# Kernel optimization log

Hardware: AMD Instinct MI355X
Metric: run time of the kernel (lower is better)

The kernel has to match this reference:

```python
import jax, jax.numpy as jnp
import numpy as np

# Module config (from init_kwargs)
RES = 64          # resolution
C = 8             # in_channels
NB = 64           # n_basis
CORE = 32         # core_size (edge of core cube on every axis)
POS = (RES - CORE) // 2  # periphery_size = 16; placement offset on each axis
DIM = CORE * CORE * CORE * C  # 262144
BATCH = 32


def setup_inputs() -> dict:
    key = jax.random.key(0)
    k_z, k_u = jax.random.split(key, 2)
    z = jax.random.normal(k_z, (BATCH, NB), dtype=jnp.float32)
    # SubspaceLayer params: U (n_basis, dim) orthogonal-init surrogate (random normal,
    # scaled like an orthonormal row basis), L = [3*n_basis, ..., 3] descending, mu zeros.
    U = jax.random.normal(k_u, (NB, DIM), dtype=jnp.float32) / np.sqrt(DIM)
    L = jnp.asarray([3.0 * i for i in range(NB, 0, -1)], dtype=jnp.float32)
    mu = jnp.zeros((DIM,), dtype=jnp.float32)
    return {"z": z, "U": U, "L": L, "mu": mu}


def reference(z, U, L, mu):
    # SubspaceLayer: (L * z) @ U + mu  -> (B, DIM)
    proj = (L * z) @ U + mu
    block = proj.reshape(-1, C, CORE, CORE, CORE)  # (B, C, 32, 32, 32)
    # einsum 'bcijk,id,jh,kw->bcdhw' with one-hot position matrices ==
    # place block into zero (B, C, RES, RES, RES) grid at offset POS per axis.
    b = block.shape[0]
    out = jnp.zeros((b, C, RES, RES, RES), dtype=block.dtype)
    out = out.at[:, :, POS:POS + CORE, POS:POS + CORE, POS:POS + CORE].set(block)
    return out
```

## Files before the change

### kernel.cpp

```cpp
#include <hip/hip_runtime.h>

#define BATCH 32
#define NB    64
#define CH    8
#define CORE  32
#define RES   64
#define POS   16
#define DIM   (CORE*CORE*CORE*CH)
#define OUT_PER_B (CH*RES*RES*RES)

#define CORE_BLOCKS (DIM/256)
#define ZERO_BLOCKS ((BATCH*OUT_PER_B/4)/256)

__global__ void prep_s_kernel(const float* __restrict__ z,
                              const float* __restrict__ L,
                              float* __restrict__ st) {
    int t = threadIdx.x;
#pragma unroll
    for (int r = 0; r < 8; ++r) {
        int idx = r * 256 + t;
        int k = idx >> 5;
        int b = idx & 31;
        st[idx] = z[b * NB + k] * L[k];
    }
}

__global__ __launch_bounds__(256) void core_part_kernel(
        const float* __restrict__ U,
        const float* __restrict__ mu,
        const float* __restrict__ st,
        float* __restrict__ out) {
    int bid = blockIdx.x;
    if (bid < CORE_BLOCKS) {
        const int d = bid * 256 + threadIdx.x;
        float acc[BATCH];
#pragma unroll
        for (int b = 0; b < BATCH; ++b) acc[b] = 0.0f;

#pragma unroll 8
        for (int k = 0; k < NB; ++k) {
            const float u = U[(size_t)k * DIM + d];
            const float* sk = st + k * BATCH;
#pragma unroll
            for (int b = 0; b < BATCH; ++b) {
                acc[b] += sk[b] * u;
            }
        }

        const float m = mu[d];
        const int c  = d >> 15;
        const int i  = (d >> 10) & 31;
        const int j  = (d >> 5) & 31;
        const int kk = d & 31;
        const size_t o = (size_t)c * (RES * RES * RES)
                       + (size_t)(i + POS) * (RES * RES)
                       + (size_t)(j + POS) * RES
                       + (size_t)(kk + POS);
#pragma unroll
        for (int b = 0; b < BATCH; ++b) {
            out[(size_t)b * OUT_PER_B + o] = acc[b] + m;
        }
    } else {
        const size_t gid4 = (size_t)(bid - CORE_BLOCKS) * 256 + threadIdx.x;
        const int rem = (int)(gid4 & 65535);
        const int i = rem >> 10;
        const int j = (rem >> 4) & 63;
        const int g = rem & 15;
        const bool in_core = (i >= POS) & (i < POS + CORE) &
                             (j >= POS) & (j < POS + CORE) &
                             (g >= 4) & (g < 12);
        if (!in_core) {
            float4* o4 = (float4*)out;
            o4[gid4] = make_float4(0.f, 0.f, 0.f, 0.f);
        }
    }
}

extern "C" void kernel_launch(void* const* d_in, const int* in_sizes, int n_in,
                              void* d_out, int out_size, void* d_ws, size_t ws_size,
                              hipStream_t stream) {
    const float* z  = (const float*)d_in[0];
    const float* U  = (const float*)d_in[1];
    const float* L  = (const float*)d_in[2];
    const float* mu = (const float*)d_in[3];
    float* out = (float*)d_out;
    float* st  = (float*)d_ws;

    prep_s_kernel<<<1, 256, 0, stream>>>(z, L, st);
    core_part_kernel<<<CORE_BLOCKS + ZERO_BLOCKS, 256, 0, stream>>>(U, mu, st, out);
}
```

Before: 323.9 us.

## Fuse scale prep into main kernel, stage in LDS, compute two outputs per thread

Removes the separate prep kernel launch by having each core block compute L*z into shared memory. Each thread now handles two adjacent columns, loading U, mu and storing output as float2. The shared scale vector is read as float4 broadcasts. This halves the core block count and cuts launch overhead, at the cost of more registers and redundant per-block scale computation.

```diff
diff --git a/kernel.cpp b/kernel.cpp
--- a/kernel.cpp
+++ b/kernel.cpp
@@ -9,56 +9,60 @@
 #define DIM   (CORE*CORE*CORE*CH)
 #define OUT_PER_B (CH*RES*RES*RES)
 
-#define CORE_BLOCKS (DIM/256)
+#define DPT   2
+#define CORE_BLOCKS (DIM/(256*DPT))
 #define ZERO_BLOCKS ((BATCH*OUT_PER_B/4)/256)
-
-__global__ void prep_s_kernel(const float* __restrict__ z,
-                              const float* __restrict__ L,
-                              float* __restrict__ st) {
-    int t = threadIdx.x;
-#pragma unroll
-    for (int r = 0; r < 8; ++r) {
-        int idx = r * 256 + t;
-        int k = idx >> 5;
-        int b = idx & 31;
-        st[idx] = z[b * NB + k] * L[k];
-    }
-}
 
 __global__ __launch_bounds__(256) void core_part_kernel(
         const float* __restrict__ U,
         const float* __restrict__ mu,
-        const float* __restrict__ st,
+        const float* __restrict__ z,
+        const float* __restrict__ L,
         float* __restrict__ out) {
-    int bid = blockIdx.x;
+    const int bid = blockIdx.x;
     if (bid < CORE_BLOCKS) {
-        const int d = bid * 256 + threadIdx.x;
-        float acc[BATCH];
+        __shared__ float st[NB * BATCH];
+        const int tid = threadIdx.x;
 #pragma unroll
-        for (int b = 0; b < BATCH; ++b) acc[b] = 0.0f;
+        for (int r = 0; r < 8; ++r) {
+            const int idx = r * 256 + tid;
+            const int k = idx >> 5;
+            const int b = idx & 31;
+            st[idx] = z[b * NB + k] * L[k];
+        }
+        __syncthreads();
 
-#pragma unroll 8
+        const int d0 = (bid * 256 + tid) * DPT;
+        float acc0[BATCH], acc1[BATCH];
+#pragma unroll
+        for (int b = 0; b < BATCH; ++b) { acc0[b] = 0.f; acc1[b] = 0.f; }
+
+#pragma unroll 2
         for (int k = 0; k < NB; ++k) {
-            const float u = U[(size_t)k * DIM + d];
-            const float* sk = st + k * BATCH;
+            const float2 u = *(const float2*)&U[(size_t)k * DIM + d0];
 #pragma unroll
-            for (int b = 0; b < BATCH; ++b) {
-                acc[b] += sk[b] * u;
+            for (int q = 0; q < 8; ++q) {
+                const float4 s = *(const float4*)&st[k * BATCH + q * 4];
+                acc0[q*4+0] += s.x * u.x;  acc1[q*4+0] += s.x * u.y;
+                acc0[q*4+1] += s.y * u.x;  acc1[q*4+1] += s.y * u.y;
+                acc0[q*4+2] += s.z * u.x;  acc1[q*4+2] += s.z * u.y;
+                acc0[q*4+3] += s.w * u.x;  acc1[q*4+3] += s.w * u.y;
             }
         }
 
-        const float m = mu[d];
-        const int c  = d >> 15;
-        const int i  = (d >> 10) & 31;
-        const int j  = (d >> 5) & 31;
-        const int kk = d & 31;
+        const float2 m = *(const float2*)&mu[d0];
+        const int c  = d0 >> 15;
+        const int i  = (d0 >> 10) & 31;
+        const int j  = (d0 >> 5) & 31;
+        const int kk = d0 & 31;
         const size_t o = (size_t)c * (RES * RES * RES)
                        + (size_t)(i + POS) * (RES * RES)
                        + (size_t)(j + POS) * RES
                        + (size_t)(kk + POS);
 #pragma unroll
         for (int b = 0; b < BATCH; ++b) {
-            out[(size_t)b * OUT_PER_B + o] = acc[b] + m;
+            float2 v = make_float2(acc0[b] + m.x, acc1[b] + m.y);
+            *(float2*)&out[(size_t)b * OUT_PER_B + o] = v;
         }
     } else {
         const size_t gid4 = (size_t)(bid - CORE_BLOCKS) * 256 + threadIdx.x;
@@ -84,8 +88,6 @@
     const float* L  = (const float*)d_in[2];
     const float* mu = (const float*)d_in[3];
     float* out = (float*)d_out;
-    float* st  = (float*)d_ws;
 
-    prep_s_kernel<<<1, 256, 0, stream>>>(z, L, st);
-    core_part_kernel<<<CORE_BLOCKS + ZERO_BLOCKS, 256, 0, stream>>>(U, mu, st, out);
+    core_part_kernel<<<CORE_BLOCKS + ZERO_BLOCKS, 256, 0, stream>>>(U, mu, z, L, out);
 }
```

Result: no change. 322.8 us (-0.3%).
